# Kernel tuning notes

Hardware: AMD Instinct MI355X
Metric: run time of the kernel (lower is better)

The kernel has to match this reference:

```python
import jax, jax.numpy as jnp
import numpy as np

N = 100000
E = 1600000
IN_C = 128
HID_C = 32
HEADS = 4
OUT_C = 64
NUM_CLASSES = 2
NUM_GRAPHS = 64
NEG_SLOPE = 0.2  # PyG GATConv default leaky_relu slope


def _segment_softmax(logits, seg, num_segments):
    # logits: [E, H], seg: [E] destination node ids
    m = jax.ops.segment_max(logits, seg, num_segments=num_segments)
    m = jnp.where(jnp.isfinite(m), m, 0.0)
    e = jnp.exp(logits - m[seg])
    s = jax.ops.segment_sum(e, seg, num_segments=num_segments)
    return e / (s[seg] + 1e-16)


def _gat_conv(x, src, dst, W, att_src, att_dst, bias, heads, ch, concat):
    n = x.shape[0]
    h = (x @ W).reshape(n, heads, ch)                 # [N, H, C]
    a_src = jnp.sum(h * att_src, axis=-1)             # [N, H]
    a_dst = jnp.sum(h * att_dst, axis=-1)             # [N, H]
    alpha = jax.nn.leaky_relu(a_src[src] + a_dst[dst], NEG_SLOPE)  # [E, H]
    alpha = _segment_softmax(alpha, dst, n)
    msg = h[src] * alpha[:, :, None]                  # [E, H, C]
    out = jax.ops.segment_sum(msg, dst, num_segments=n)  # [N, H, C]
    out = out.reshape(n, heads * ch) if concat else out.mean(axis=1)
    return out + bias


def setup_inputs() -> dict:
    key = jax.random.key(0)
    ks = jax.random.split(key, 12)
    x = jax.random.normal(ks[0], (N, IN_C), dtype=jnp.float32)
    edge_index = jax.random.randint(ks[1], (2, E), 0, N, dtype=jnp.int32)
    batch = jnp.sort(jax.random.randint(ks[2], (N,), 0, NUM_GRAPHS, dtype=jnp.int32))
    s1 = 1.0 / np.sqrt(IN_C)
    W1 = jax.random.uniform(ks[3], (IN_C, HEADS * HID_C), minval=-s1, maxval=s1, dtype=jnp.float32)
    att_src1 = jax.random.normal(ks[4], (HEADS, HID_C), dtype=jnp.float32) * 0.1
    att_dst1 = jax.random.normal(ks[5], (HEADS, HID_C), dtype=jnp.float32) * 0.1
    b1 = jnp.zeros((HEADS * HID_C,), dtype=jnp.float32)
    s2 = 1.0 / np.sqrt(HEADS * HID_C)
    W2 = jax.random.uniform(ks[6], (HEADS * HID_C, OUT_C), minval=-s2, maxval=s2, dtype=jnp.float32)
    att_src2 = jax.random.normal(ks[7], (1, OUT_C), dtype=jnp.float32) * 0.1
    att_dst2 = jax.random.normal(ks[8], (1, OUT_C), dtype=jnp.float32) * 0.1
    b2 = jnp.zeros((OUT_C,), dtype=jnp.float32)
    sc = 1.0 / np.sqrt(OUT_C)
    Wc = jax.random.uniform(ks[9], (OUT_C, NUM_CLASSES), minval=-sc, maxval=sc, dtype=jnp.float32)
    bc = jnp.zeros((NUM_CLASSES,), dtype=jnp.float32)
    return {"x": x, "edge_index": edge_index, "batch": batch,
            "W1": W1, "att_src1": att_src1, "att_dst1": att_dst1, "b1": b1,
            "W2": W2, "att_src2": att_src2, "att_dst2": att_dst2, "b2": b2,
            "Wc": Wc, "bc": bc}


def reference(x, edge_index, batch, W1, att_src1, att_dst1, b1,
              W2, att_src2, att_dst2, b2, Wc, bc):
    # PyG GATConv adds self-loops by default
    loops = jnp.arange(N, dtype=edge_index.dtype)
    src = jnp.concatenate([edge_index[0], loops])
    dst = jnp.concatenate([edge_index[1], loops])
    # eval mode: dropout is identity
    h = _gat_conv(x, src, dst, W1, att_src1, att_dst1, b1, HEADS, HID_C, True)
    h = jax.nn.elu(h)
    h = _gat_conv(h, src, dst, W2, att_src2, att_dst2, b2, 1, OUT_C, False)
    h = jax.nn.elu(h)
    # global mean pool over graphs
    sums = jax.ops.segment_sum(h, batch, num_segments=NUM_GRAPHS)
    cnts = jax.ops.segment_sum(jnp.ones((N, 1), h.dtype), batch, num_segments=NUM_GRAPHS)
    pooled = sums / jnp.maximum(cnts, 1.0)
    return pooled @ Wc + bc
```

## Files before the change

kernel.cpp:

```cpp
#include <hip/hip_runtime.h>
#include <math.h>


typedef __attribute__((ext_vector_type(8))) short bf16x8;
typedef __attribute__((ext_vector_type(4))) float f32x4;

__device__ __forceinline__ unsigned f2bf_rne(float x){
  unsigned u = __float_as_uint(x);
  return (u + 0x7fffu + ((u >> 16) & 1u)) >> 16;
}
__device__ __forceinline__ unsigned pk_bf2(float a, float b){
  return f2bf_rne(a) | (f2bf_rne(b) << 16);
}
__device__ __forceinline__ void unpack8(uint4 q, float* f){
  f[0] = __uint_as_float(q.x << 16);
  f[1] = __uint_as_float(q.x & 0xffff0000u);
  f[2] = __uint_as_float(q.y << 16);
  f[3] = __uint_as_float(q.y & 0xffff0000u);
  f[4] = __uint_as_float(q.z << 16);
  f[5] = __uint_as_float(q.z & 0xffff0000u);
  f[6] = __uint_as_float(q.w << 16);
  f[7] = __uint_as_float(q.w & 0xffff0000u);
}


#define CHUNKE 8192

__global__ __launch_bounds__(256) void k_bucketcount(
    const int* __restrict__ dst, int* __restrict__ bcnt, int e, int NB)
{
  __shared__ int hcnt[512];
  const int tid = threadIdx.x;
  for (int b = tid; b < 512; b += 256) hcnt[b] = 0;
  __syncthreads();
  const int lo = blockIdx.x * CHUNKE;
  const int hi = min(lo + CHUNKE, e);
  for (int i = lo + tid; i < hi; i += 256)
    atomicAdd(&hcnt[dst[i] >> 8], 1);
  __syncthreads();
  for (int b = tid; b < NB; b += 256)
    if (hcnt[b]) atomicAdd(&bcnt[b], hcnt[b]);
}

__global__ __launch_bounds__(512) void k_bucketscan(
    const int* __restrict__ bcnt, int* __restrict__ bbase,
    int* __restrict__ cur, int* __restrict__ off, int e, int n, int NB,
    const float* __restrict__ W1, const float* __restrict__ as1w,
    const float* __restrict__ ad1w,
    const float* __restrict__ W2, const float* __restrict__ as2w,
    const float* __restrict__ ad2w,
    unsigned short* __restrict__ wa1, unsigned short* __restrict__ wa2)
{
  const int t = threadIdx.x;

  if (blockIdx.x == 1){
    for (int i = t; i < 2048; i += 512) wa2[i] = 0;
    __syncthreads();
    {
      int k = t >> 2, j = t & 3;
      float ds = 0.f, dd = 0.f;
      for (int cc = 0; cc < 32; ++cc){
        float wv = W1[k * 128 + j * 32 + cc];
        ds = fmaf(wv, as1w[j * 32 + cc], ds);
        dd = fmaf(wv, ad1w[j * 32 + cc], dd);
      }
      unsigned hs_ = f2bf_rne(ds); float hsf = __uint_as_float(hs_ << 16);
      unsigned ls_ = f2bf_rne(ds - hsf);
      unsigned hd_ = f2bf_rne(dd); float hdf = __uint_as_float(hd_ << 16);
      unsigned ld_ = f2bf_rne(dd - hdf);
      wa1[(j     ) * 128 + k] = (unsigned short)hs_;
      wa1[(j + 4 ) * 128 + k] = (unsigned short)ls_;
      wa1[(j + 8 ) * 128 + k] = (unsigned short)hd_;
      wa1[(j + 12) * 128 + k] = (unsigned short)ld_;
    }
    if (t < 128){
      int k = t;
      float ds = 0.f, dd = 0.f;
      for (int cc = 0; cc < 64; ++cc){
        float wv = W2[k * 64 + cc];
        ds = fmaf(wv, as2w[cc], ds);
        dd = fmaf(wv, ad2w[cc], dd);
      }
      unsigned hs_ = f2bf_rne(ds); float hsf = __uint_as_float(hs_ << 16);
      unsigned ls_ = f2bf_rne(ds - hsf);
      unsigned hd_ = f2bf_rne(dd); float hdf = __uint_as_float(hd_ << 16);
      unsigned ld_ = f2bf_rne(dd - hdf);
      wa2[ 0 * 128 + k] = (unsigned short)hs_;
      wa2[ 4 * 128 + k] = (unsigned short)ls_;
      wa2[ 8 * 128 + k] = (unsigned short)hd_;
      wa2[12 * 128 + k] = (unsigned short)ld_;
    }
    return;
  }

  __shared__ int sh[512];
  int v = (t < NB) ? bcnt[t] : 0;
  sh[t] = v;
  __syncthreads();
  for (int o = 1; o < 512; o <<= 1){
    int x = (t >= o) ? sh[t - o] : 0;
    __syncthreads();
    sh[t] += x;
    __syncthreads();
  }
  if (t < NB){
    int excl = sh[t] - v;
    bbase[t] = excl;
    cur[t]   = excl;
  }
  if (t == 0) off[n] = e;
}

__global__ __launch_bounds__(256) void k_partition(
    const int* __restrict__ src, const int* __restrict__ dst,
    int* __restrict__ cur, unsigned* __restrict__ packed, int e, int NB)
{
  __shared__ unsigned       recs[CHUNKE];
  __shared__ unsigned short bkt[CHUNKE];
  __shared__ int hcnt[512];
  __shared__ int hoff[512];
  __shared__ int hbase[512];

  const int tid = threadIdx.x;
  const int lo  = blockIdx.x * CHUNKE;
  const int hi  = min(lo + CHUNKE, e);
  const int cnt = hi - lo;

  hcnt[tid] = 0; hcnt[tid + 256] = 0;
  __syncthreads();
  for (int i = lo + tid; i < hi; i += 256)
    atomicAdd(&hcnt[dst[i] >> 8], 1);
  __syncthreads();

  hoff[tid] = hcnt[tid]; hoff[tid + 256] = hcnt[tid + 256];
  __syncthreads();
  for (int o = 1; o < 512; o <<= 1){
    int x0 = (tid >= o)       ? hoff[tid - o]       : 0;
    int x1 = (tid + 256 >= o) ? hoff[tid + 256 - o] : 0;
    __syncthreads();
    hoff[tid] += x0; hoff[tid + 256] += x1;
    __syncthreads();
  }

  int c0 = hcnt[tid], c1 = hcnt[tid + 256];
  int e0 = hoff[tid] - c0, e1 = hoff[tid + 256] - c1;
  hbase[tid]       = c0 ? atomicAdd(&cur[tid], c0)       : 0;
  hbase[tid + 256] = c1 ? atomicAdd(&cur[tid + 256], c1) : 0;
  __syncthreads();
  hoff[tid] = e0; hoff[tid + 256] = e1;
  hcnt[tid] = 0;  hcnt[tid + 256] = 0;
  __syncthreads();

  for (int i = lo + tid; i < hi; i += 256){
    int d = dst[i];
    int b = d >> 8;
    int p = hoff[b] + atomicAdd(&hcnt[b], 1);
    recs[p] = (unsigned)src[i] | ((unsigned)(d & 255) << 17);
    bkt[p]  = (unsigned short)b;
  }
  __syncthreads();

  for (int t = tid; t < cnt; t += 256){
    int b = bkt[t];
    packed[hbase[b] + t - hoff[b]] = recs[t];
  }
}

__global__ __launch_bounds__(256) void k_bucketbuild(
    const unsigned* __restrict__ packed, const int* __restrict__ bbase,
    const int* __restrict__ bcnt, int* __restrict__ off,
    int* __restrict__ csr, int n)
{
  __shared__ int lcnt[256];
  __shared__ int loff[256];
  const int b    = blockIdx.x;
  const int tid  = threadIdx.x;
  const int seg0 = bbase[b];
  const int scnt = bcnt[b];

  lcnt[tid] = 0;
  __syncthreads();
  for (int i = tid; i < scnt; i += 256)
    atomicAdd(&lcnt[packed[seg0 + i] >> 17], 1);
  __syncthreads();
  int v = lcnt[tid];
  loff[tid] = v;
  __syncthreads();
  for (int o = 1; o < 256; o <<= 1){
    int x = (tid >= o) ? loff[tid - o] : 0;
    __syncthreads();
    loff[tid] += x;
    __syncthreads();
  }
  int excl = loff[tid] - v;
  __syncthreads();
  loff[tid] = excl;
  lcnt[tid] = 0;
  int d = (b << 8) + tid;
  if (d < n) off[d] = seg0 + excl;
  __syncthreads();
  for (int i = tid; i < scnt; i += 256){
    unsigned rec = packed[seg0 + i];
    int doff = rec >> 17;
    int s    = rec & 0x1FFFF;
    int p    = atomicAdd(&lcnt[doff], 1);
    csr[seg0 + loff[doff] + p] = s;
  }
}


template<int OUTC, int HEADS, bool XBF16, typename XT>
__global__ __launch_bounds__(256) void k_gemm_mfma(
    const XT* __restrict__ X, const float* __restrict__ W,
    const unsigned short* __restrict__ WATT,
    unsigned short* __restrict__ H, float* __restrict__ ASRC,
    float* __restrict__ ADST, int n)
{
  constexpr int K  = 128;
  constexpr int KC = 32;
  constexpr int CT = OUTC / 16;
  constexpr int CTX = CT + 1;
  constexpr int RT = 16 / CT;
  constexpr int WROWS = RT * 16;
  constexpr int BROWS = WROWS * 4;

  __shared__ unsigned short Bs[OUTC + 16][K + 8];
  __shared__ unsigned short As[BROWS][KC + 8];

  const int tid   = threadIdx.x;
  const int lane  = tid & 63;
  const int c15   = lane & 15;
  const int quad  = lane >> 4;
  const int warow = (tid >> 6) * WROWS;
  const int row0  = blockIdx.x * BROWS;

  f32x4 acc[CTX][RT];
  #pragma unroll
  for (int ct = 0; ct < CTX; ++ct)
    #pragma unroll
    for (int t = 0; t < RT; ++t)
      #pragma unroll
      for (int r = 0; r < 4; ++r) acc[ct][t][r] = 0.f;

  for (int idx = tid; idx < K * OUTC / 4; idx += 256){
    int k  = idx / (OUTC / 4);
    int c4 = (idx % (OUTC / 4)) * 4;
    float4 v = *(const float4*)&W[(size_t)k * OUTC + c4];
    Bs[c4 + 0][k] = (unsigned short)f2bf_rne(v.x);
    Bs[c4 + 1][k] = (unsigned short)f2bf_rne(v.y);
    Bs[c4 + 2][k] = (unsigned short)f2bf_rne(v.z);
    Bs[c4 + 3][k] = (unsigned short)f2bf_rne(v.w);
  }
  for (int idx = tid; idx < 16 * (K / 8); idx += 256){
    int rr = idx >> 4;
    int q  = idx & 15;
    *(uint4*)&Bs[OUTC + rr][q * 8] = *(const uint4*)&WATT[rr * K + q * 8];
  }

  for (int kc = 0; kc < K; kc += KC){
    if (XBF16){
      for (int idx = tid; idx < BROWS * (KC / 8); idx += 256){
        int rr = idx / (KC / 8);
        int q  = idx % (KC / 8);
        int row = row0 + rr;
        uint4 v = make_uint4(0, 0, 0, 0);
        if (row < n) v = *(const uint4*)((const unsigned short*)X + (size_t)row * K + kc + q * 8);
        *(uint4*)&As[rr][q * 8] = v;
      }
    } else {
      for (int idx = tid; idx < BROWS * (KC / 4); idx += 256){
        int rr = idx / (KC / 4);
        int q  = idx % (KC / 4);
        int row = row0 + rr;
        float4 v = make_float4(0.f, 0.f, 0.f, 0.f);
        if (row < n) v = *(const float4*)((const float*)X + (size_t)row * K + kc + q * 4);
        *(uint2*)&As[rr][q * 4] = make_uint2(pk_bf2(v.x, v.y), pk_bf2(v.z, v.w));
      }
    }
    __syncthreads();

    bf16x8 af[RT];
    #pragma unroll
    for (int t = 0; t < RT; ++t)
      af[t] = *(const bf16x8*)&As[warow + t * 16 + c15][8 * quad];
    #pragma unroll
    for (int ct = 0; ct < CTX; ++ct){
      bf16x8 bfr = *(const bf16x8*)&Bs[ct * 16 + c15][kc + 8 * quad];
      #pragma unroll
      for (int t = 0; t < RT; ++t)
        acc[ct][t] = __builtin_amdgcn_mfma_f32_16x16x32_bf16(af[t], bfr, acc[ct][t], 0, 0, 0);
    }
    __syncthreads();
  }

  #pragma unroll
  for (int t = 0; t < RT; ++t){
    #pragma unroll
    for (int r = 0; r < 4; ++r){
      int row = row0 + warow + t * 16 + quad * 4 + r;
      float av = acc[CT][t][r];
      av += __shfl_xor(av, 4);
      if (row < n){
        #pragma unroll
        for (int ct = 0; ct < CT; ++ct)
          H[(size_t)row * OUTC + ct * 16 + c15] = (unsigned short)f2bf_rne(acc[ct][t][r]);
        if (c15 < HEADS)                      ASRC[row * HEADS + c15] = av;
        else if (c15 >= 8 && c15 < 8 + HEADS) ADST[row * HEADS + c15 - 8] = av;
      }
    }
  }
}


template<int CH, int HEADS, bool OUTBF16, int DSTS>
__global__ __launch_bounds__(256) void k_aggregate(
    const unsigned short* __restrict__ Hmsg, const float* __restrict__ ASRC,
    const float* __restrict__ ADST, const int* __restrict__ off,
    const int* __restrict__ csr, const float* __restrict__ bias,
    void* __restrict__ OUT, int n)
{
  constexpr int CL  = CH / 8;
  constexpr int GPB = 256 / CL;
  constexpr int CPH = CH / HEADS;
  constexpr int RQ  = CH / 8;

  const int tid = threadIdx.x;
  const int cl  = tid % CL;
  const int c0  = cl * 8;
  const int h   = c0 / CPH;
  const int g   = blockIdx.x * GPB + tid / CL;
  const uint4* Hv = (const uint4*)Hmsg;

  float bv[8];
  #pragma unroll
  for (int j = 0; j < 8; ++j) bv[j] = bias[c0 + j];

  #pragma unroll 1
  for (int it = 0; it < DSTS; ++it){
    const int d = g * DSTS + it;
    if (d >= n) break;

    const float adst = ADST[d * HEADS + h];

    float acc[8];
    float wsum;
    {
      float t = ASRC[d * HEADS + h] + adst;
      float w = __expf(fmaxf(t, 0.2f * t));
      float f[8];
      unpack8(Hv[d * RQ + cl], f);
      #pragma unroll
      for (int j = 0; j < 8; ++j) acc[j] = w * f[j];
      wsum = w;
    }

    const int s0   = off[d];
    const int cnt  = off[d + 1] - s0;
    const int full = cnt & ~7;

    for (int p = 0; p < full; p += 8){
      int idx[8];
      #pragma unroll
      for (int j = 0; j < 8; ++j) idx[j] = csr[s0 + p + j];
      float av[8];
      #pragma unroll
      for (int j = 0; j < 8; ++j) av[j] = ASRC[idx[j] * HEADS + h];
      uint4 hq[8];
      #pragma unroll
      for (int j = 0; j < 8; ++j) hq[j] = Hv[idx[j] * RQ + cl];
      #pragma unroll
      for (int j = 0; j < 8; ++j){
        float t = av[j] + adst;
        float w = __expf(fmaxf(t, 0.2f * t));
        float f[8];
        unpack8(hq[j], f);
        #pragma unroll
        for (int q = 0; q < 8; ++q) acc[q] = fmaf(w, f[q], acc[q]);
        wsum += w;
      }
    }

    const int rem = cnt - full;
    if (rem){
      int  idx[8];
      bool ok[8];
      #pragma unroll
      for (int j = 0; j < 8; ++j){
        int q = csr[s0 + full + j];
        ok[j]  = j < rem;
        idx[j] = ok[j] ? q : 0;
      }
      float av[8];
      #pragma unroll
      for (int j = 0; j < 8; ++j) av[j] = ASRC[idx[j] * HEADS + h];
      uint4 hq[8];
      #pragma unroll
      for (int j = 0; j < 8; ++j) hq[j] = Hv[idx[j] * RQ + cl];
      #pragma unroll
      for (int j = 0; j < 8; ++j){
        float t = av[j] + adst;
        float w = __expf(fmaxf(t, 0.2f * t));
        w = ok[j] ? w : 0.f;
        float f[8];
        unpack8(hq[j], f);
        #pragma unroll
        for (int q = 0; q < 8; ++q) acc[q] = fmaf(w, f[q], acc[q]);
        wsum += w;
      }
    }

    const float inv = 1.f / (wsum + 1e-16f);
    float o[8];
    #pragma unroll
    for (int j = 0; j < 8; ++j){
      float v = acc[j] * inv + bv[j];
      o[j] = v > 0.f ? v : expm1f(v);
    }
    if (OUTBF16){
      uint4 q;
      q.x = pk_bf2(o[0], o[1]); q.y = pk_bf2(o[2], o[3]);
      q.z = pk_bf2(o[4], o[5]); q.w = pk_bf2(o[6], o[7]);
      *(uint4*)((unsigned short*)OUT + (size_t)d * CH + c0) = q;
    } else {
      float* Of = (float*)OUT;
      *(float4*)&Of[(size_t)d * CH + c0 + 0] = make_float4(o[0], o[1], o[2], o[3]);
      *(float4*)&Of[(size_t)d * CH + c0 + 4] = make_float4(o[4], o[5], o[6], o[7]);
    }
  }
}


__global__ __launch_bounds__(256) void k_pool_partial(
    const float* __restrict__ H, const int* __restrict__ batch,
    float* __restrict__ sums, int n)
{
  constexpr int CHUNK = 256;
  const int c    = threadIdx.x & 63;
  const int slot = threadIdx.x >> 6;
  const int start = blockIdx.x * CHUNK;
  const int end   = min(start + CHUNK, n);

  float acc = 0.f;
  int cur = -1;
  for (int nn = start + slot; nn < end; nn += 4){
    int g = batch[nn];
    if (g != cur){
      if (cur >= 0) atomicAdd(&sums[cur * 64 + c], acc);
      acc = 0.f; cur = g;
    }
    acc += H[(size_t)nn * 64 + c];
  }
  if (cur >= 0) atomicAdd(&sums[cur * 64 + c], acc);
}

__global__ __launch_bounds__(128) void k_classify(
    const float* __restrict__ sums, const int* __restrict__ batch,
    const float* __restrict__ Wc, const float* __restrict__ bc,
    float* __restrict__ out, int n)
{
  int t = threadIdx.x;
  if (t >= 128) return;
  int g = t >> 1, cls = t & 1;
  int lo = 0, hi = n;
  while (lo < hi){ int m = (lo + hi) >> 1; if (batch[m] < g) lo = m + 1; else hi = m; }
  int s = lo;
  lo = s; hi = n;
  while (lo < hi){ int m = (lo + hi) >> 1; if (batch[m] < g + 1) lo = m + 1; else hi = m; }
  int cnt = lo - s;
  float inv = 1.f / (float)(cnt > 1 ? cnt : 1);
  float dot = 0.f;
  #pragma unroll
  for (int c = 0; c < 64; ++c) dot = fmaf(sums[g * 64 + c], Wc[c * 2 + cls], dot);
  out[g * 2 + cls] = dot * inv + bc[cls];
}


extern "C" void kernel_launch(void* const* d_in, const int* in_sizes, int n_in,
                              void* d_out, int out_size, void* d_ws, size_t ws_size,
                              hipStream_t stream)
{
  const float* x    = (const float*)d_in[0];
  const int*   edge = (const int*)  d_in[1];
  const int*   batch= (const int*)  d_in[2];
  const float* W1   = (const float*)d_in[3];
  const float* as1w = (const float*)d_in[4];
  const float* ad1w = (const float*)d_in[5];
  const float* b1   = (const float*)d_in[6];
  const float* W2   = (const float*)d_in[7];
  const float* as2w = (const float*)d_in[8];
  const float* ad2w = (const float*)d_in[9];
  const float* b2   = (const float*)d_in[10];
  const float* Wc   = (const float*)d_in[11];
  const float* bc   = (const float*)d_in[12];

  const int n = in_sizes[2];
  const int e = in_sizes[1] / 2;
  const int* esrc = edge;
  const int* edst = edge + e;
  const int NB = (n + 255) >> 8;

  unsigned short* h1  = (unsigned short*)d_ws;
  unsigned short* h1a = h1 + (size_t)n * 128;
  float* as1 = (float*)(h1a + (size_t)n * 128);
  float* ad1 = as1 + (size_t)n * 4;
  float* as2 = ad1 + (size_t)n * 4;
  float* ad2 = as2 + (size_t)n;
  float* sums = ad2 + (size_t)n;
  unsigned short* wa1 = (unsigned short*)(sums + 64 * 64);
  unsigned short* wa2 = wa1 + 2048;
  int*  bcnt  = (int*)(wa2 + 2048);
  int*  cur   = bcnt + 512;
  int*  bbase = cur + 512;
  int*  off   = bbase + 512;
  unsigned* packed = (unsigned*)(off + n + 1);
  int*  csr   = (int*)(packed + e);

  const int eb = (e + CHUNKE - 1) / CHUNKE;

  hipMemsetAsync(sums, 0, 64 * 64 * 4 + 2 * 4096 + 512 * 4, stream);
  k_bucketcount<<<eb, 256, 0, stream>>>(edst, bcnt, e, NB);
  k_bucketscan <<<2, 512, 0, stream>>>(bcnt, bbase, cur, off, e, n, NB,
                                       W1, as1w, ad1w, W2, as2w, ad2w, wa1, wa2);
  k_partition  <<<eb, 256, 0, stream>>>(esrc, edst, cur, packed, e, NB);
  k_bucketbuild<<<NB, 256, 0, stream>>>(packed, bbase, bcnt, off, csr, n);

  k_gemm_mfma<128, 4, false><<<(n + 127) / 128, 256, 0, stream>>>(
      x, W1, wa1, h1, as1, ad1, n);
  k_aggregate<128, 4, true, 4><<<(n + 63) / 64, 256, 0, stream>>>(
      h1, as1, ad1, off, csr, b1, (void*)h1a, n);

  unsigned short* h2 = h1;
  float* h2a = (float*)h1a;
  k_gemm_mfma<64, 1, true><<<(n + 255) / 256, 256, 0, stream>>>(
      h1a, W2, wa2, h2, as2, ad2, n);
  k_aggregate<64, 1, false, 4><<<(n + 127) / 128, 256, 0, stream>>>(
      h2, as2, ad2, off, csr, b2, (void*)h2a, n);

  k_pool_partial<<<(n + 255) / 256, 256, 0, stream>>>(h2a, batch, sums, n);
  k_classify<<<1, 128, 0, stream>>>(sums, batch, Wc, bc, (float*)d_out, n);
}
```

Before: 375.9 us.

## Fuse mean-pool into second aggregation and use one destination per thread group

The global mean-pool partial sums move into the second GAT aggregation kernel. Each block reduces its outputs into shared-memory per-graph accumulators and then issues global atomics, so the fp32 node-feature write and the separate pool kernel go away. Both aggregation launches also change from four destinations per thread group to one, giving more blocks and more parallelism for the latency-bound gather. The cost is shared-memory atomics and a block barrier in the pooled kernel, plus more blocks overall.

```diff
diff --git a/kernel.cpp b/kernel.cpp
--- a/kernel.cpp
+++ b/kernel.cpp
@@ -312,34 +312,37 @@
 }
 
 
-template<int CH, int HEADS, bool OUTBF16, int DSTS>
+template<int CH, int HEADS, bool OUTBF16, bool POOL>
 __global__ __launch_bounds__(256) void k_aggregate(
     const unsigned short* __restrict__ Hmsg, const float* __restrict__ ASRC,
     const float* __restrict__ ADST, const int* __restrict__ off,
     const int* __restrict__ csr, const float* __restrict__ bias,
-    void* __restrict__ OUT, int n)
+    void* __restrict__ OUT, const int* __restrict__ batch,
+    float* __restrict__ gsums, int n)
 {
   constexpr int CL  = CH / 8;
   constexpr int GPB = 256 / CL;
   constexpr int CPH = CH / HEADS;
   constexpr int RQ  = CH / 8;
 
+  __shared__ float lsum[POOL ? 256 : 1];
+
   const int tid = threadIdx.x;
   const int cl  = tid % CL;
   const int c0  = cl * 8;
   const int h   = c0 / CPH;
-  const int g   = blockIdx.x * GPB + tid / CL;
+  const int d   = (int)blockIdx.x * GPB + tid / CL;
   const uint4* Hv = (const uint4*)Hmsg;
 
-  float bv[8];
-  #pragma unroll
-  for (int j = 0; j < 8; ++j) bv[j] = bias[c0 + j];
-
-  #pragma unroll 1
-  for (int it = 0; it < DSTS; ++it){
-    const int d = g * DSTS + it;
-    if (d >= n) break;
-
+  int gbase = 0;
+  if (POOL){
+    int probe = (int)blockIdx.x * GPB;
+    gbase = batch[probe < n - 1 ? probe : n - 1];
+    lsum[tid] = 0.f;
+    __syncthreads();
+  }
+
+  if (d < n){
     const float adst = ADST[d * HEADS + h];
 
     float acc[8];
@@ -413,10 +416,20 @@
     float o[8];
     #pragma unroll
     for (int j = 0; j < 8; ++j){
-      float v = acc[j] * inv + bv[j];
+      float v = acc[j] * inv + bias[c0 + j];
       o[j] = v > 0.f ? v : expm1f(v);
     }
-    if (OUTBF16){
+    if (POOL){
+      int gb  = batch[d];
+      int rel = gb - gbase;
+      if (rel >= 0 && rel < 4){
+        #pragma unroll
+        for (int j = 0; j < 8; ++j) atomicAdd(&lsum[rel * 64 + c0 + j], o[j]);
+      } else {
+        #pragma unroll
+        for (int j = 0; j < 8; ++j) atomicAdd(&gsums[gb * 64 + c0 + j], o[j]);
+      }
+    } else if (OUTBF16){
       uint4 q;
       q.x = pk_bf2(o[0], o[1]); q.y = pk_bf2(o[2], o[3]);
       q.z = pk_bf2(o[4], o[5]); q.w = pk_bf2(o[6], o[7]);
@@ -427,30 +440,16 @@
       *(float4*)&Of[(size_t)d * CH + c0 + 4] = make_float4(o[4], o[5], o[6], o[7]);
     }
   }
-}
-
-
-__global__ __launch_bounds__(256) void k_pool_partial(
-    const float* __restrict__ H, const int* __restrict__ batch,
-    float* __restrict__ sums, int n)
-{
-  constexpr int CHUNK = 256;
-  const int c    = threadIdx.x & 63;
-  const int slot = threadIdx.x >> 6;
-  const int start = blockIdx.x * CHUNK;
-  const int end   = min(start + CHUNK, n);
-
-  float acc = 0.f;
-  int cur = -1;
-  for (int nn = start + slot; nn < end; nn += 4){
-    int g = batch[nn];
-    if (g != cur){
-      if (cur >= 0) atomicAdd(&sums[cur * 64 + c], acc);
-      acc = 0.f; cur = g;
-    }
-    acc += H[(size_t)nn * 64 + c];
-  }
-  if (cur >= 0) atomicAdd(&sums[cur * 64 + c], acc);
+
+  if (POOL){
+    __syncthreads();
+    int slot = tid >> 6;
+    int ch   = tid & 63;
+    float v = lsum[slot * 64 + ch];
+    int gg = gbase + slot;
+    if (v != 0.f && gg < 64)
+      atomicAdd(&gsums[gg * 64 + ch], v);
+  }
 }
 
 __global__ __launch_bounds__(128) void k_classify(
@@ -517,7 +516,7 @@
 
   const int eb = (e + CHUNKE - 1) / CHUNKE;
 
-  hipMemsetAsync(sums, 0, 64 * 64 * 4 + 2 * 4096 + 512 * 4, stream);
+  (void)hipMemsetAsync(sums, 0, 64 * 64 * 4 + 2 * 4096 + 512 * 4, stream);
   k_bucketcount<<<eb, 256, 0, stream>>>(edst, bcnt, e, NB);
   k_bucketscan <<<2, 512, 0, stream>>>(bcnt, bbase, cur, off, e, n, NB,
                                        W1, as1w, ad1w, W2, as2w, ad2w, wa1, wa2);
@@ -526,16 +525,14 @@
 
   k_gemm_mfma<128, 4, false><<<(n + 127) / 128, 256, 0, stream>>>(
       x, W1, wa1, h1, as1, ad1, n);
-  k_aggregate<128, 4, true, 4><<<(n + 63) / 64, 256, 0, stream>>>(
-      h1, as1, ad1, off, csr, b1, (void*)h1a, n);
+  k_aggregate<128, 4, true, false><<<(n + 15) / 16, 256, 0, stream>>>(
+      h1, as1, ad1, off, csr, b1, (void*)h1a, nullptr, nullptr, n);
 
   unsigned short* h2 = h1;
-  float* h2a = (float*)h1a;
   k_gemm_mfma<64, 1, true><<<(n + 255) / 256, 256, 0, stream>>>(
       h1a, W2, wa2, h2, as2, ad2, n);
-  k_aggregate<64, 1, false, 4><<<(n + 127) / 128, 256, 0, stream>>>(
-      h2, as2, ad2, off, csr, b2, (void*)h2a, n);
-
-  k_pool_partial<<<(n + 255) / 256, 256, 0, stream>>>(h2a, batch, sums, n);
+  k_aggregate<64, 1, false, true><<<(n + 31) / 32, 256, 0, stream>>>(
+      h2, as2, ad2, off, csr, b2, nullptr, batch, sums, n);
+
   k_classify<<<1, 128, 0, stream>>>(sums, batch, Wc, bc, (float*)d_out, n);
 }
```

Result: no change. 380.0 us (+1.1%).
